# Optimization experiments

Measured on AMD Instinct MI355X. Metric: run time of the kernel, lower is better.

## Reference

```python
import jax, jax.numpy as jnp
import numpy as np

N_NODES = 100000
N_EDGES = 3200000
F_IN, F_HID, F_OUT = 36, 8, 2
NEG_SLOPE = 0.2


def gat_layer(x, src, dst, W, a_src, a_dst, b, num_nodes):
    # Linear transform: [N, F'] 
    h = x @ W
    # Per-node attention logits (heads=1)
    alpha_s = h @ a_src  # [N]
    alpha_d = h @ a_dst  # [N]
    # Edge-wise score: leaky_relu(a_src . h_j + a_dst . h_i) for edge j->i
    e = jax.nn.leaky_relu(alpha_s[src] + alpha_d[dst], negative_slope=NEG_SLOPE)  # [E]
    # Segment softmax over incoming edges of each dst node
    m = jax.ops.segment_max(e, dst, num_segments=num_nodes)  # [N]
    ee = jnp.exp(e - m[dst])
    denom = jax.ops.segment_sum(ee, dst, num_segments=num_nodes)  # [N]
    alpha = ee / denom[dst]  # [E]
    # Scatter-aggregate messages
    out = jax.ops.segment_sum(alpha[:, None] * h[src], dst, num_segments=num_nodes)
    return out + b


def setup_inputs() -> dict:
    key = jax.random.key(0)
    ks = jax.random.split(key, 10)
    x = jax.random.normal(ks[0], (N_NODES, F_IN), dtype=jnp.float32)
    edge_index = jax.random.randint(ks[1], (2, N_EDGES), 0, N_NODES, dtype=jnp.int64)
    s1 = 1.0 / np.sqrt(F_IN)
    s2 = 1.0 / np.sqrt(F_HID)
    W1 = jax.random.uniform(ks[2], (F_IN, F_HID), jnp.float32, -s1, s1)
    a_src1 = jax.random.uniform(ks[3], (F_HID,), jnp.float32, -s2, s2)
    a_dst1 = jax.random.uniform(ks[4], (F_HID,), jnp.float32, -s2, s2)
    b1 = jnp.zeros((F_HID,), jnp.float32)
    W2 = jax.random.uniform(ks[5], (F_HID, F_OUT), jnp.float32, -s2, s2)
    so = 1.0 / np.sqrt(F_OUT)
    a_src2 = jax.random.uniform(ks[6], (F_OUT,), jnp.float32, -so, so)
    a_dst2 = jax.random.uniform(ks[7], (F_OUT,), jnp.float32, -so, so)
    b2 = jnp.zeros((F_OUT,), jnp.float32)
    return {"x": x, "edge_index": edge_index, "W1": W1, "a_src1": a_src1,
            "a_dst1": a_dst1, "b1": b1, "W2": W2, "a_src2": a_src2,
            "a_dst2": a_dst2, "b2": b2}


def reference(x, edge_index, W1, a_src1, a_dst1, b1, W2, a_src2, a_dst2, b2):
    src, dst = edge_index[0], edge_index[1]
    n = x.shape[0]
    h = jax.nn.relu(gat_layer(x, src, dst, W1, a_src1, a_dst1, b1, n))
    # dropout is identity in eval mode
    out = gat_layer(h, src, dst, W2, a_src2, a_dst2, b2, n)
    return jax.nn.log_softmax(out, axis=1)
```

## Files before the change

kernel.cpp:

```cpp
#include <hip/hip_runtime.h>
#include <hip/hip_bf16.h>

#define N_NODES 100000
#define N_EDGES 3200000
#define F_IN 36
#define F_HID 8
#define F_OUT 2
#define NEG_SLOPE 0.2f

#define GSHIFT 7
#define GNPB 128
#define GNBUCK 782
#define CAP 4608
#define NB_PART 256
#define CHUNK 12500
#define BP 1024
#define BPG 512

__device__ __forceinline__ int detect_is64(const void* eidx, int* s_flag) {
    if (threadIdx.x < 64) {
        const unsigned int* p = (const unsigned int*)eidx;
        unsigned int v1 = p[2 * threadIdx.x + 1];
        unsigned int v2 = p[2 * (threadIdx.x + 64) + 1];
        unsigned long long m = __ballot(v1 != 0u || v2 != 0u);
        if (threadIdx.x == 0) *s_flag = (m == 0ull) ? 1 : 0;
    }
    __syncthreads();
    return *s_flag;
}

__global__ void partition1_k(const void* __restrict__ eidx, int* __restrict__ gcnt,
                             int* __restrict__ partP) {
    __shared__ int h[GNBUCK];
    __shared__ int s_flag;
    int t = threadIdx.x;
    for (int i = t; i < GNBUCK; i += BP) h[i] = 0;
    int f = detect_is64(eidx, &s_flag);
    int beg = blockIdx.x * CHUNK;
    int end = beg + CHUNK; if (end > N_EDGES) end = N_EDGES;
    if (f) {
        const long long* p = (const long long*)eidx;
        for (int i = beg + t; i < end; i += BP) atomicAdd(&h[(int)p[N_EDGES + i] >> GSHIFT], 1);
    } else {
        const int* p = (const int*)eidx;
        for (int i = beg + t; i < end; i += BP) atomicAdd(&h[p[N_EDGES + i] >> GSHIFT], 1);
    }
    __syncthreads();
    for (int i = t; i < GNBUCK; i += BP) {
        int c = h[i];
        h[i] = c ? atomicAdd(&gcnt[i], c) : 0;
    }
    __syncthreads();
    if (f) {
        const long long* p = (const long long*)eidx;
        for (int i = beg + t; i < end; i += BP) {
            int s = (int)p[i];
            int d = (int)p[N_EDGES + i];
            int b = d >> GSHIFT;
            int pos = atomicAdd(&h[b], 1);
            if (pos < CAP) partP[b * CAP + pos] = (s << GSHIFT) | (d & (GNPB - 1));
        }
    } else {
        const int* p = (const int*)eidx;
        for (int i = beg + t; i < end; i += BP) {
            int s = p[i];
            int d = p[N_EDGES + i];
            int b = d >> GSHIFT;
            int pos = atomicAdd(&h[b], 1);
            if (pos < CAP) partP[b * CAP + pos] = (s << GSHIFT) | (d & (GNPB - 1));
        }
    }
}

__global__ void node1_k(const float* __restrict__ x, const float* __restrict__ W1,
                        const float* __restrict__ aw_s, const float* __restrict__ aw_d,
                        float* __restrict__ h1, float* __restrict__ as1, float* __restrict__ ad1,
                        int n_nodes) {
    int n = blockIdx.x * blockDim.x + threadIdx.x;
    if (n >= n_nodes) return;
    float acc[F_HID];
#pragma unroll
    for (int f = 0; f < F_HID; f++) acc[f] = 0.f;
    const float4* xp = (const float4*)(x + (size_t)n * F_IN);
#pragma unroll
    for (int q = 0; q < 9; q++) {
        float4 xv = xp[q];
        const float* w = W1 + q * 4 * F_HID;
#pragma unroll
        for (int f = 0; f < F_HID; f++) {
            acc[f] += xv.x * w[0 * F_HID + f] + xv.y * w[1 * F_HID + f]
                    + xv.z * w[2 * F_HID + f] + xv.w * w[3 * F_HID + f];
        }
    }
    float s = 0.f, d = 0.f;
#pragma unroll
    for (int f = 0; f < F_HID; f++) {
        s += acc[f] * aw_s[f];
        d += acc[f] * aw_d[f];
    }
    float4* hp = (float4*)(h1 + (size_t)n * F_HID);
    hp[0] = make_float4(acc[0], acc[1], acc[2], acc[3]);
    hp[1] = make_float4(acc[4], acc[5], acc[6], acc[7]);
    as1[n] = s;
    ad1[n] = d;
}

__global__ void gatF1_k(const int* __restrict__ gcnt, const int* __restrict__ partP,
                        int* __restrict__ e_srcP, int2* __restrict__ rowinfo,
                        const float* __restrict__ as1, const float* __restrict__ ad1,
                        const float* __restrict__ h1, const float* __restrict__ b1,
                        const float* __restrict__ W2, const float* __restrict__ aw_s2,
                        const float* __restrict__ aw_d2, float4* __restrict__ P2) {
    __shared__ int eL[CAP];
    __shared__ int hist[GNPB];
    __shared__ int nstart[GNPB];
    __shared__ int cursor[GNPB];
    __shared__ int sscan[GNPB];
    __shared__ float adl[GNPB];
    int t = threadIdx.x;
    int c = blockIdx.x;
    int nbase = c << GSHIFT;
    int beg = c * CAP;
    int cnt = gcnt[c]; if (cnt > CAP) cnt = CAP;

    if (t < GNPB) {
        hist[t] = 0;
        adl[t] = (nbase + t < N_NODES) ? ad1[nbase + t] : 0.f;
    }
    __syncthreads();
    for (int j = t; j < cnt; j += BPG)
        atomicAdd(&hist[partP[beg + j] & (GNPB - 1)], 1);
    __syncthreads();
    if (t < GNPB) sscan[t] = hist[t];
    __syncthreads();
    for (int o = 1; o < GNPB; o <<= 1) {
        int u = (t < GNPB && t >= o) ? sscan[t - o] : 0;
        __syncthreads();
        if (t < GNPB) sscan[t] += u;
        __syncthreads();
    }
    if (t < GNPB) {
        int ex = sscan[t] - hist[t];
        nstart[t] = ex;
        cursor[t] = ex;
        int node = nbase + t;
        if (node < N_NODES) rowinfo[node] = make_int2(beg + ex, hist[t]);
    }
    __syncthreads();
    for (int j = t; j < cnt; j += BPG) {
        int pk = partP[beg + j];
        int pos = atomicAdd(&cursor[pk & (GNPB - 1)], 1);
        eL[pos] = pk >> GSHIFT;
    }
    __syncthreads();
    for (int i = t; i < cnt; i += BPG) e_srcP[beg + i] = eL[i];

    int node = t >> 2;
    int lane = t & 3;
    int gnode = nbase + node;
    if (gnode >= N_NODES) return;
    int ns = nstart[node];
    int ne = ns + hist[node];
    float add = adl[node];

    float denom = 0.f;
    float acc[F_HID];
#pragma unroll
    for (int f = 0; f < F_HID; f++) acc[f] = 0.f;
    for (int i = ns + lane; i < ne; i += 4) {
        int s = eL[i];
        float e = as1[s] + add;
        e = e >= 0.f ? e : NEG_SLOPE * e;
        float ee = __expf(e);
        denom += ee;
        const float4* hp = (const float4*)(h1 + (size_t)s * F_HID);
        float4 p0 = hp[0], p1 = hp[1];
        acc[0] += ee * p0.x; acc[1] += ee * p0.y; acc[2] += ee * p0.z; acc[3] += ee * p0.w;
        acc[4] += ee * p1.x; acc[5] += ee * p1.y; acc[6] += ee * p1.z; acc[7] += ee * p1.w;
    }
#pragma unroll
    for (int o = 2; o > 0; o >>= 1) {
        denom += __shfl_xor(denom, o, 4);
#pragma unroll
        for (int f = 0; f < F_HID; f++) acc[f] += __shfl_xor(acc[f], o, 4);
    }
    if (lane == 0) {
        float inv = denom > 0.f ? 1.f / denom : 0.f;
        float o0 = 0.f, o1 = 0.f;
#pragma unroll
        for (int f = 0; f < F_HID; f++) {
            float v = acc[f] * inv + b1[f];
            v = v > 0.f ? v : 0.f;
            o0 += v * W2[f * F_OUT + 0];
            o1 += v * W2[f * F_OUT + 1];
        }
        float as2v = o0 * aw_s2[0] + o1 * aw_s2[1];
        float ad2v = o0 * aw_d2[0] + o1 * aw_d2[1];
        P2[gnode] = make_float4(as2v, o0, o1, ad2v);
    }
}

__global__ void gat2_k(const int2* __restrict__ rowinfo, const int* __restrict__ e_srcP,
                       const float4* __restrict__ P2, const float* __restrict__ b2,
                       float* __restrict__ out, int n_nodes) {
    int gid = blockIdx.x * 16 + (threadIdx.x >> 4);
    int lane = threadIdx.x & 15;
    if (gid >= n_nodes) return;
    int2 ri = rowinfo[gid];
    float add = P2[gid].w;

    float denom = 0.f, a0 = 0.f, a1 = 0.f;
    int jend = ri.x + ri.y;
    for (int j = ri.x + lane; j < jend; j += 16) {
        int s = e_srcP[j];
        float4 q = P2[s];
        float e = q.x + add;
        e = e >= 0.f ? e : NEG_SLOPE * e;
        float ee = __expf(e);
        denom += ee;
        a0 += ee * q.y;
        a1 += ee * q.z;
    }
#pragma unroll
    for (int o = 8; o > 0; o >>= 1) {
        denom += __shfl_xor(denom, o, 16);
        a0 += __shfl_xor(a0, o, 16);
        a1 += __shfl_xor(a1, o, 16);
    }

    if (lane == 0) {
        float inv = denom > 0.f ? 1.f / denom : 0.f;
        float o0 = a0 * inv + b2[0];
        float o1 = a1 * inv + b2[1];
        float M = fmaxf(o0, o1);
        float l = M + logf(__expf(o0 - M) + __expf(o1 - M));
        ((float2*)out)[gid] = make_float2(o0 - l, o1 - l);
    }
}

extern "C" void kernel_launch(void* const* d_in, const int* in_sizes, int n_in,
                              void* d_out, int out_size, void* d_ws, size_t ws_size,
                              hipStream_t stream) {
    const float* x      = (const float*)d_in[0];
    const void*  eidx   = d_in[1];
    const float* W1     = (const float*)d_in[2];
    const float* a_src1 = (const float*)d_in[3];
    const float* a_dst1 = (const float*)d_in[4];
    const float* b1     = (const float*)d_in[5];
    const float* W2     = (const float*)d_in[6];
    const float* a_src2 = (const float*)d_in[7];
    const float* a_dst2 = (const float*)d_in[8];
    const float* b2     = (const float*)d_in[9];
    float* out = (float*)d_out;

    const size_t N = N_NODES;
    const size_t PADDED = (size_t)GNBUCK * CAP;

    int* wsi = (int*)d_ws;
    float* wsf = (float*)d_ws;
    size_t o = 0;
    int* partP    = wsi + o;      o += PADDED;
    int* e_srcP   = wsi + o;      o += PADDED;
    int* gcnt     = wsi + o;      o += 800;
    int2* rowinfo = (int2*)(wsi + o); o += 2 * N;
    float* as1    = wsf + o;      o += N;
    float* ad1    = wsf + o;      o += N;
    float* h1     = wsf + o;      o += 8 * N;
    float4* P2    = (float4*)(wsf + o); o += 4 * N;

    const int B = 256;
    const int gridN = (int)((N + B - 1) / B);
    const int gridG = (int)(N / 16);

    hipMemsetAsync(gcnt, 0, 800 * sizeof(int), stream);

    partition1_k<<<NB_PART, BP, 0, stream>>>(eidx, gcnt, partP);
    node1_k<<<gridN, B, 0, stream>>>(x, W1, a_src1, a_dst1, h1, as1, ad1, (int)N);
    gatF1_k<<<GNBUCK, BPG, 0, stream>>>(gcnt, partP, e_srcP, rowinfo, as1, ad1, h1, b1,
                                        W2, a_src2, a_dst2, P2);
    gat2_k<<<gridG, B, 0, stream>>>(rowinfo, e_srcP, P2, b2, out, (int)N);
}
```

Baseline: 183.9 us.

## Locally sort edges by bucket in LDS before coalesced scatter to partitions

The partition kernel now counting-sorts each chunk of edges by destination bucket in shared memory, using a block-wide prefix scan over bucket histograms. Each thread then finds its element's bucket with a binary search and writes it out, so consecutive threads write contiguous runs within a bucket instead of scattering randomly to global memory. It also reads only the low 32-bit words of int64 indices. The cost is about 60KB of LDS per block, extra scan syncs, and a binary search per element.

New measurement: 184.3 us. No clear change (+0.2%).

```diff
diff --git a/kernel.cpp b/kernel.cpp
--- a/kernel.cpp
+++ b/kernel.cpp
@@ -31,34 +31,50 @@
 
 __global__ void partition1_k(const void* __restrict__ eidx, int* __restrict__ gcnt,
                              int* __restrict__ partP) {
-    __shared__ int h[GNBUCK];
+    __shared__ int sortbuf[CHUNK];
+    __shared__ int hist[GNBUCK];
+    __shared__ int spre[GNBUCK];
+    __shared__ int cursor[GNBUCK];
+    __shared__ int gbase[GNBUCK];
     __shared__ int s_flag;
     int t = threadIdx.x;
-    for (int i = t; i < GNBUCK; i += BP) h[i] = 0;
+    for (int i = t; i < GNBUCK; i += BP) hist[i] = 0;
     int f = detect_is64(eidx, &s_flag);
     int beg = blockIdx.x * CHUNK;
     int end = beg + CHUNK; if (end > N_EDGES) end = N_EDGES;
+    int cnt = end - beg;
+    const unsigned int* p32 = (const unsigned int*)eidx;
     if (f) {
-        const long long* p = (const long long*)eidx;
-        for (int i = beg + t; i < end; i += BP) atomicAdd(&h[(int)p[N_EDGES + i] >> GSHIFT], 1);
+        for (int i = beg + t; i < end; i += BP)
+            atomicAdd(&hist[(int)p32[2 * (N_EDGES + i)] >> GSHIFT], 1);
     } else {
         const int* p = (const int*)eidx;
-        for (int i = beg + t; i < end; i += BP) atomicAdd(&h[p[N_EDGES + i] >> GSHIFT], 1);
-    }
-    __syncthreads();
-    for (int i = t; i < GNBUCK; i += BP) {
-        int c = h[i];
-        h[i] = c ? atomicAdd(&gcnt[i], c) : 0;
-    }
+        for (int i = beg + t; i < end; i += BP)
+            atomicAdd(&hist[p[N_EDGES + i] >> GSHIFT], 1);
+    }
+    __syncthreads();
+    if (t < GNBUCK) {
+        int c = hist[t];
+        gbase[t] = c ? atomicAdd(&gcnt[t], c) : 0;
+        spre[t] = c;
+    }
+    __syncthreads();
+    for (int off = 1; off < GNBUCK; off <<= 1) {
+        int v = 0;
+        if (t < GNBUCK && t >= off) v = spre[t - off];
+        __syncthreads();
+        if (t < GNBUCK && t >= off) spre[t] += v;
+        __syncthreads();
+    }
+    if (t < GNBUCK) cursor[t] = spre[t] - hist[t];
     __syncthreads();
     if (f) {
-        const long long* p = (const long long*)eidx;
         for (int i = beg + t; i < end; i += BP) {
-            int s = (int)p[i];
-            int d = (int)p[N_EDGES + i];
+            int s = (int)p32[2 * i];
+            int d = (int)p32[2 * (N_EDGES + i)];
             int b = d >> GSHIFT;
-            int pos = atomicAdd(&h[b], 1);
-            if (pos < CAP) partP[b * CAP + pos] = (s << GSHIFT) | (d & (GNPB - 1));
+            int pos = atomicAdd(&cursor[b], 1);
+            sortbuf[pos] = (s << GSHIFT) | (d & (GNPB - 1));
         }
     } else {
         const int* p = (const int*)eidx;
@@ -66,9 +82,20 @@
             int s = p[i];
             int d = p[N_EDGES + i];
             int b = d >> GSHIFT;
-            int pos = atomicAdd(&h[b], 1);
-            if (pos < CAP) partP[b * CAP + pos] = (s << GSHIFT) | (d & (GNPB - 1));
-        }
+            int pos = atomicAdd(&cursor[b], 1);
+            sortbuf[pos] = (s << GSHIFT) | (d & (GNPB - 1));
+        }
+    }
+    __syncthreads();
+    for (int i = t; i < cnt; i += BP) {
+        int lo = 0, hi = GNBUCK - 1;
+        while (lo < hi) {
+            int mid = (lo + hi) >> 1;
+            if (spre[mid] > i) hi = mid; else lo = mid + 1;
+        }
+        int b = lo;
+        int gp = gbase[b] + (i - (spre[b] - hist[b]));
+        if (gp < CAP) partP[b * CAP + gp] = sortbuf[i];
     }
 }
 
```
